# Performance work log

Hardware: AMD Instinct MI355X
Metric: run time of the kernel (lower is better)

Reference implementation:

```python
import jax, jax.numpy as jnp
import numpy as np

EPS = 1e-5
SCALE_MIN, SCALE_MAX = 0.6, 1.0


def _layer_norm(x):
    m = jnp.mean(x, axis=-1, keepdims=True)
    v = jnp.mean((x - m) ** 2, axis=-1, keepdims=True)
    return (x - m) / jnp.sqrt(v + EPS)


def _scan_dir(seq, A, Bp, Cp, D, W_in, W_out, snr_scale):
    """seq: [B, L, C] -> [B, L, C]. Diagonal SSM recurrence h = A*h + B*u."""
    Bsz, L, C = seq.shape
    N = A.shape[0]
    seq = _layer_norm(seq)
    u = jnp.einsum('blc,nc->bln', seq, W_in)                 # input_proj, [B,L,N]
    A_base = jnp.tanh(A)[None, :]                            # [1,N]
    s = jnp.clip(snr_scale, 0.0, 1.0)[:, None]               # [B,1]
    scale = SCALE_MIN + (SCALE_MAX - SCALE_MIN) * s
    Ad = jnp.clip(A_base * scale, -0.99, 0.99)               # [B,N]
    Bu = Bp[None, None, :] * u                               # [B,L,N]

    def step(h, bu_t):
        h = Ad * h + bu_t
        return h, h

    h0 = jnp.zeros((Bsz, N), dtype=seq.dtype)
    _, hs = jax.lax.scan(step, h0, jnp.swapaxes(Bu, 0, 1))   # hs: [L,B,N]
    hs = jnp.swapaxes(hs, 0, 1)                              # [B,L,N]
    y_state = Cp[None, None, :] * hs
    y = jnp.einsum('bln,cn->blc', y_state, W_out)            # output_proj
    return y + D[None, None, :] * seq


def _forward(x, snr_scale, A, Bparam, Cparam, D, W_in, W_out):
    Bsz, H, W, C = x.shape
    L = H * W
    if L > 4000:
        x = _layer_norm(x)
    # row scans
    seq_row = x.reshape(Bsz, L, C)
    y_row_f = _scan_dir(seq_row, A, Bparam, Cparam, D, W_in, W_out, snr_scale)
    y_row_b = _scan_dir(seq_row[:, ::-1, :], A, Bparam, Cparam, D, W_in, W_out, snr_scale)
    y_row = 0.5 * (y_row_f + y_row_b[:, ::-1, :])
    y_row = y_row.reshape(Bsz, H, W, C)
    # column scans
    x_col = jnp.transpose(x, (0, 2, 1, 3))                   # [B,W,H,C]
    seq_col = x_col.reshape(Bsz, L, C)
    y_col_f = _scan_dir(seq_col, A, Bparam, Cparam, D, W_in, W_out, snr_scale)
    y_col_b = _scan_dir(seq_col[:, ::-1, :], A, Bparam, Cparam, D, W_in, W_out, snr_scale)
    y_col = 0.5 * (y_col_f + y_col_b[:, ::-1, :])
    y_col = jnp.transpose(y_col.reshape(Bsz, W, H, C), (0, 2, 1, 3))
    return 0.5 * (y_row + y_col)


def setup_inputs() -> dict:
    key = jax.random.key(0)
    k = jax.random.split(key, 4)
    Bsz, H, W, C, N = 8, 64, 64, 256, 64
    x = jax.random.normal(k[0], (Bsz, H, W, C), dtype=jnp.float32)
    snr_scale = jax.random.uniform(k[1], (Bsz,), dtype=jnp.float32)
    A = -0.5 * jnp.ones((N,), dtype=jnp.float32)
    Bparam = 0.5 * jnp.ones((N,), dtype=jnp.float32)
    Cparam = 0.5 * jnp.ones((N,), dtype=jnp.float32)
    D = jnp.zeros((C,), dtype=jnp.float32)
    # nn.Linear default init: U(-1/sqrt(fan_in), 1/sqrt(fan_in))
    W_in = jax.random.uniform(k[2], (N, C), dtype=jnp.float32,
                              minval=-1.0 / np.sqrt(C), maxval=1.0 / np.sqrt(C))
    W_out = jax.random.uniform(k[3], (C, N), dtype=jnp.float32,
                               minval=-1.0 / np.sqrt(N), maxval=1.0 / np.sqrt(N))
    return {"x": x, "snr_scale": snr_scale, "A": A, "Bparam": Bparam,
            "Cparam": Cparam, "D": D, "W_in": W_in, "W_out": W_out}


def reference(x, snr_scale, A, Bparam, Cparam, D, W_in, W_out):
    return _forward(x, snr_scale, A, Bparam, Cparam, D, W_in, W_out)
```

## Files before the change

### kernel.cpp

```cpp
#include <hip/hip_runtime.h>
#include <hip/hip_bf16.h>
#include <math.h>

#define Bsz 8
#define Hh 64
#define Ww 64
#define Cc 256
#define Nn 64
#define Ll 4096
#define EPSf 1e-5f

typedef __bf16 v8bf __attribute__((ext_vector_type(8)));
typedef float  f32x4 __attribute__((ext_vector_type(4)));

__device__ __forceinline__ float ad_val(float a, float snr) {
    float s = fminf(fmaxf(snr, 0.f), 1.f);
    float scale = 0.6f + 0.4f * s;
    float v = tanhf(a) * scale;
    return fminf(fmaxf(v, -0.99f), 0.99f);
}

__global__ __launch_bounds__(256) void k0_weights(
    const float* __restrict__ Win, const float* __restrict__ Wout,
    const float* __restrict__ Bp, const float* __restrict__ Cp,
    __bf16* __restrict__ Wh, __bf16* __restrict__ Wl,
    __bf16* __restrict__ Woh, __bf16* __restrict__ Wol,
    float* __restrict__ WB)
{
    const int t = threadIdx.x;
    const int blk = blockIdx.x;
    if (blk < 4) {
        for (int idx = blk * 512 + t; idx < blk * 512 + 512; idx += 256) {
            int tile = idx >> 6, lane = idx & 63;
            int kt = tile >> 2, nt = tile & 3;
            int q = lane >> 4, n = nt * 16 + (lane & 15);
            #pragma unroll
            for (int j = 0; j < 8; ++j) {
                int k = kt * 32 + q * 8 + j;
                float w = Win[n * Cc + k];
                __bf16 h = (__bf16)w;
                Wh[idx * 8 + j] = h;
                Wl[idx * 8 + j] = (__bf16)(w - (float)h);
            }
        }
    } else if (blk < 8) {
        for (int idx = (blk - 4) * 512 + t; idx < (blk - 4) * 512 + 512; idx += 256) {
            int tile = idx >> 6, lane = idx & 63;
            int kt = tile >> 4, ntg = tile & 15;
            int q = lane >> 4, c = ntg * 16 + (lane & 15);
            #pragma unroll
            for (int j = 0; j < 8; ++j) {
                int k = kt * 32 + q * 8 + j;
                float w = Wout[c * Nn + k] * 0.25f * Cp[k];
                __bf16 h = (__bf16)w;
                Woh[idx * 8 + j] = h;
                Wol[idx * 8 + j] = (__bf16)(w - (float)h);
            }
        }
    } else {
        __shared__ float wtmp[256];
        int n = t >> 2, qd = t & 3;
        float s = 0.f;
        const float* wr = Win + (long)n * Cc + qd * 64;
        for (int i = 0; i < 64; ++i) s += wr[i];
        wtmp[t] = s;
        __syncthreads();
        if (t < 64)
            WB[t] = (wtmp[t*4] + wtmp[t*4+1] + wtmp[t*4+2] + wtmp[t*4+3]) * Bp[t];
    }
}

__global__ __launch_bounds__(256) void k1_ln_gemm(
    const float* __restrict__ x, const __bf16* __restrict__ Wh,
    const __bf16* __restrict__ Wl, const float* __restrict__ Bp,
    const float* __restrict__ WB, float* __restrict__ Bu,
    float* __restrict__ Mst, float* __restrict__ Sst)
{
    __shared__ float mrow[64], srow[64];
    const int t = threadIdx.x;
    const int lane = t & 63;
    const int wv = __builtin_amdgcn_readfirstlane(t >> 6);
    const long pbase = (long)blockIdx.x * 64;
    const float* xt = x + pbase * Cc;

    for (int rr = 0; rr < 16; ++rr) {
        int r = wv * 16 + rr;
        float4 v = ((const float4*)(xt + (long)r * Cc))[lane];
        float s = v.x + v.y + v.z + v.w;
        float q = v.x*v.x + v.y*v.y + v.z*v.z + v.w*v.w;
        #pragma unroll
        for (int off = 32; off > 0; off >>= 1) {
            s += __shfl_down(s, off);
            q += __shfl_down(q, off);
        }
        if (lane == 0) {
            float m = s * (1.f/256.f);
            float var = fmaxf(q * (1.f/256.f) - m*m, 0.f);
            float r1 = rsqrtf(var + EPSf);
            float v2 = var / (var + EPSf);
            float sc = r1 * rsqrtf(v2 + EPSf);
            mrow[r] = m; srow[r] = sc;
            Mst[pbase + r] = m; Sst[pbase + r] = sc;
        }
    }
    __syncthreads();

    const int q = lane >> 4;
    const int mi = lane & 15;
    const float* xa = xt + (long)(wv * 16 + mi) * Cc + q * 8;

    f32x4 acc[4];
    #pragma unroll
    for (int nt = 0; nt < 4; ++nt) acc[nt] = (f32x4){0.f, 0.f, 0.f, 0.f};

    #pragma unroll
    for (int kt = 0; kt < 8; ++kt) {
        float4 a0 = *(const float4*)(xa + kt * 32);
        float4 a1 = *(const float4*)(xa + kt * 32 + 4);
        float av[8] = {a0.x, a0.y, a0.z, a0.w, a1.x, a1.y, a1.z, a1.w};
        v8bf ah, al;
        #pragma unroll
        for (int j = 0; j < 8; ++j) {
            __bf16 h = (__bf16)av[j];
            ah[j] = h;
            al[j] = (__bf16)(av[j] - (float)h);
        }
        #pragma unroll
        for (int nt = 0; nt < 4; ++nt) {
            v8bf bh = *(const v8bf*)(Wh + ((long)(kt * 4 + nt) * 64 + lane) * 8);
            v8bf bl = *(const v8bf*)(Wl + ((long)(kt * 4 + nt) * 64 + lane) * 8);
            acc[nt] = __builtin_amdgcn_mfma_f32_16x16x32_bf16(ah, bh, acc[nt], 0, 0, 0);
            acc[nt] = __builtin_amdgcn_mfma_f32_16x16x32_bf16(al, bh, acc[nt], 0, 0, 0);
            acc[nt] = __builtin_amdgcn_mfma_f32_16x16x32_bf16(ah, bl, acc[nt], 0, 0, 0);
        }
    }

    #pragma unroll
    for (int nt = 0; nt < 4; ++nt) {
        int n = nt * 16 + mi;
        float bpn = Bp[n];
        float wbn = WB[n];
        #pragma unroll
        for (int reg = 0; reg < 4; ++reg) {
            int p = wv * 16 + q * 4 + reg;
            float m = mrow[p], s = srow[p];
            Bu[(pbase + p) * Nn + n] = s * (acc[nt][reg] * bpn - m * wbn);
        }
    }
}

__global__ __launch_bounds__(256) void k2_carry(
    const float* __restrict__ Bu, const float* __restrict__ A,
    const float* __restrict__ snr, float* __restrict__ E)
{
    const int t = threadIdx.x;
    const int lane = t & 63;
    const int task = blockIdx.x * 4 + (t >> 6);
    const int isCol = task >> 9;
    const int b = (task >> 6) & 7;
    const int j = task & 63;
    const float Ad = ad_val(A[lane], snr[b]);
    const float* src = Bu + ((long)b * Ll + (isCol ? j : j * 64)) * Nn + lane;
    const long stride = isCol ? (long)Ww * Nn : Nn;

    float v[64];
    #pragma unroll
    for (int k = 0; k < 64; ++k) v[k] = src[k * stride];

    float s = 0.f;
    #pragma unroll
    for (int k = 0; k < 64; ++k) s = fmaf(Ad, s, v[k]);
    const int dF = isCol ? 2 : 0;
    E[((dF * 8 + b) * 64 + j) * 64 + lane] = s;

    float sb = 0.f;
    #pragma unroll
    for (int k = 63; k >= 0; --k) sb = fmaf(Ad, sb, v[k]);
    E[(((dF + 1) * 8 + b) * 64 + (63 - j)) * 64 + lane] = sb;
}

__global__ __launch_bounds__(64) void k3_prefix(
    const float* __restrict__ E, float* __restrict__ CT,
    const float* __restrict__ A, const float* __restrict__ snr)
{
    const int lane = threadIdx.x;
    const int db = blockIdx.x;
    const int b = db & 7;
    float Ad = ad_val(A[lane], snr[b]);
    float p64 = Ad;
    #pragma unroll
    for (int i = 0; i < 6; ++i) p64 *= p64;
    const float* e = E + (long)db * 4096 + lane;
    float* ct = CT + (long)db * 4096 + lane;
    float v[64];
    #pragma unroll
    for (int k = 0; k < 64; ++k) v[k] = e[k * 64];
    float c = 0.f;
    #pragma unroll
    for (int k = 0; k < 64; ++k) {
        ct[k * 64] = c;
        c = fmaf(p64, c, v[k]);
    }
}

__global__ __launch_bounds__(256) void k4_apply(
    const float* __restrict__ Bu, const float* __restrict__ CT,
    const float* __restrict__ A, const float* __restrict__ snr,
    float* __restrict__ Srow, float* __restrict__ Scol)
{
    const int t = threadIdx.x;
    const int lane = t & 63;
    const int task = blockIdx.x * 4 + (t >> 6);
    const int isCol = task >> 9;
    const int b = (task >> 6) & 7;
    const int j = task & 63;
    const float Ad = ad_val(A[lane], snr[b]);
    const float* src = Bu + ((long)b * Ll + (isCol ? j : j * 64)) * Nn + lane;
    const long stride = isCol ? (long)Ww * Nn : Nn;
    const int dF = isCol ? 2 : 0;
    const float cf = CT[((dF * 8 + b) * 64 + j) * 64 + lane];
    const float cb = CT[(((dF + 1) * 8 + b) * 64 + (63 - j)) * 64 + lane];

    float v[64];
    #pragma unroll
    for (int k = 0; k < 64; ++k) v[k] = src[k * stride];

    float hf[64];
    float h = cf;
    #pragma unroll
    for (int k = 0; k < 64; ++k) { h = fmaf(Ad, h, v[k]); hf[k] = h; }

    float* out0 = (isCol ? Scol : Srow) +
                  ((long)b * Ll + (isCol ? j : j * 64)) * Nn + lane;
    float sb = cb;
    #pragma unroll
    for (int k = 63; k >= 0; --k) {
        sb = fmaf(Ad, sb, v[k]);
        out0[k * stride] = hf[k] + sb;
    }
}

__global__ __launch_bounds__(256) void k5_gemm_out(
    const float* __restrict__ Srow, const float* __restrict__ Scol,
    const float* __restrict__ x, const __bf16* __restrict__ Woh,
    const __bf16* __restrict__ Wol, const float* __restrict__ Dp,
    const float* __restrict__ Mst, const float* __restrict__ Sst,
    float* __restrict__ out)
{
    __shared__ float smem[64 * 260];
    const int t = threadIdx.x;
    const int lane = t & 63;
    const int wv = __builtin_amdgcn_readfirstlane(t >> 6);
    const long pbase = (long)blockIdx.x * 64;
    const int q = lane >> 4;
    const int mi = lane & 15;

    const float4* Sr = (const float4*)(Srow + pbase * Nn);
    const float4* Sc = (const float4*)(Scol + pbase * Nn);
    #pragma unroll
    for (int i = 0; i < 4; ++i) {
        int fi = i * 256 + t;
        float4 a = Sr[fi], c = Sc[fi];
        *(float4*)&smem[(fi >> 4) * 68 + (fi & 15) * 4] =
            make_float4(a.x + c.x, a.y + c.y, a.z + c.z, a.w + c.w);
    }
    __syncthreads();

    f32x4 acc[4][4];
    #pragma unroll
    for (int mt = 0; mt < 4; ++mt)
        #pragma unroll
        for (int nt = 0; nt < 4; ++nt) acc[mt][nt] = (f32x4){0.f, 0.f, 0.f, 0.f};

    #pragma unroll
    for (int kt = 0; kt < 2; ++kt) {
        v8bf bh[4], bl[4];
        #pragma unroll
        for (int nt = 0; nt < 4; ++nt) {
            long wo = ((long)(kt * 16 + wv * 4 + nt) * 64 + lane) * 8;
            bh[nt] = *(const v8bf*)(Woh + wo);
            bl[nt] = *(const v8bf*)(Wol + wo);
        }
        #pragma unroll
        for (int mt = 0; mt < 4; ++mt) {
            const float* ar = &smem[(mt * 16 + mi) * 68 + q * 8 + kt * 32];
            v8bf sh, sl;
            #pragma unroll
            for (int j = 0; j < 8; ++j) {
                float sv = ar[j];
                __bf16 hh = (__bf16)sv;
                sh[j] = hh;
                sl[j] = (__bf16)(sv - (float)hh);
            }
            #pragma unroll
            for (int nt = 0; nt < 4; ++nt) {
                acc[mt][nt] = __builtin_amdgcn_mfma_f32_16x16x32_bf16(sh, bh[nt], acc[mt][nt], 0, 0, 0);
                acc[mt][nt] = __builtin_amdgcn_mfma_f32_16x16x32_bf16(sl, bh[nt], acc[mt][nt], 0, 0, 0);
                acc[mt][nt] = __builtin_amdgcn_mfma_f32_16x16x32_bf16(sh, bl[nt], acc[mt][nt], 0, 0, 0);
            }
        }
    }
    __syncthreads();
    #pragma unroll
    for (int mt = 0; mt < 4; ++mt)
        #pragma unroll
        for (int nt = 0; nt < 4; ++nt) {
            int c = wv * 64 + nt * 16 + mi;
            #pragma unroll
            for (int reg = 0; reg < 4; ++reg)
                smem[(mt * 16 + q * 4 + reg) * 260 + c] = acc[mt][nt][reg];
        }
    __syncthreads();

    const float4* xg = (const float4*)(x + pbase * Cc);
    float4* og = (float4*)(out + pbase * Cc);
    const float4 dv = ((const float4*)Dp)[lane];
    #pragma unroll 4
    for (int i = 0; i < 16; ++i) {
        int fi = i * 256 + t;
        int p = i * 4 + wv;
        float4 v = *(const float4*)&smem[p * 260 + lane * 4];
        float m = Mst[pbase + p], s = Sst[pbase + p];
        float4 xv = xg[fi];
        og[fi] = make_float4(v.x + dv.x * ((xv.x - m) * s),
                             v.y + dv.y * ((xv.y - m) * s),
                             v.z + dv.z * ((xv.z - m) * s),
                             v.w + dv.w * ((xv.w - m) * s));
    }
}

extern "C" void kernel_launch(void* const* d_in, const int* in_sizes, int n_in,
                              void* d_out, int out_size, void* d_ws, size_t ws_size,
                              hipStream_t stream)
{
    const float* x    = (const float*)d_in[0];
    const float* snr  = (const float*)d_in[1];
    const float* A    = (const float*)d_in[2];
    const float* Bp   = (const float*)d_in[3];
    const float* Cp   = (const float*)d_in[4];
    const float* Dp   = (const float*)d_in[5];
    const float* Win  = (const float*)d_in[6];
    const float* Wout = (const float*)d_in[7];
    float* out = (float*)d_out;

    char* ws = (char*)d_ws;
    float*  Bu   = (float*)(ws);
    float*  Srow = (float*)(ws + (size_t)8  * 1024 * 1024);
    float*  Scol = (float*)(ws + (size_t)16 * 1024 * 1024);
    float*  E    = (float*)(ws + (size_t)24 * 1024 * 1024);
    float*  CT   = (float*)(ws + (size_t)24 * 1024 * 1024 + 512*1024);
    float*  Mst  = (float*)(ws + (size_t)25 * 1024 * 1024);
    float*  Sst  = (float*)(ws + (size_t)25 * 1024 * 1024 + 128*1024);
    char*   wbase = ws + (size_t)25 * 1024 * 1024 + 512 * 1024;
    __bf16* Wh   = (__bf16*)(wbase);
    __bf16* Wl   = (__bf16*)(wbase + 32 * 1024);
    __bf16* Woh  = (__bf16*)(wbase + 64 * 1024);
    __bf16* Wol  = (__bf16*)(wbase + 96 * 1024);
    float*  WB   = (float*)(wbase + 128 * 1024);

    hipLaunchKernelGGL(k0_weights,  dim3(9),   dim3(256), 0, stream, Win, Wout, Bp, Cp, Wh, Wl, Woh, Wol, WB);
    hipLaunchKernelGGL(k1_ln_gemm,  dim3(512), dim3(256), 0, stream, x, Wh, Wl, Bp, WB, Bu, Mst, Sst);
    hipLaunchKernelGGL(k2_carry,    dim3(256), dim3(256), 0, stream, Bu, A, snr, E);
    hipLaunchKernelGGL(k3_prefix,   dim3(32),  dim3(64),  0, stream, E, CT, A, snr);
    hipLaunchKernelGGL(k4_apply,    dim3(256), dim3(256), 0, stream, Bu, CT, A, snr, Srow, Scol);
    hipLaunchKernelGGL(k5_gemm_out, dim3(512), dim3(256), 0, stream, Srow, Scol, x, Woh, Wol, Dp, Mst, Sst, out);
}
```

Before: 140.8 us.

## Fuse row-scan carry into LN-GEMM and row-scan apply into output GEMM

Row-direction scan chunk carries are now computed inside k1 from the Bu tile held in LDS, using a 4-segment split per 64-row chunk. The row-direction apply is moved into k5, which rebuilds the row scan from Bu plus the prefix carries and adds the column result before the output GEMM. This removes the Srow buffer and its 8 MB write and read, and halves the k2 and k4 grids to column-only work. In exchange k1 and k5 take extra LDS, barriers and sequential per-segment recurrence work.

```diff
diff --git a/kernel.cpp b/kernel.cpp
--- a/kernel.cpp
+++ b/kernel.cpp
@@ -73,10 +73,14 @@
 __global__ __launch_bounds__(256) void k1_ln_gemm(
     const float* __restrict__ x, const __bf16* __restrict__ Wh,
     const __bf16* __restrict__ Wl, const float* __restrict__ Bp,
-    const float* __restrict__ WB, float* __restrict__ Bu,
+    const float* __restrict__ WB, const float* __restrict__ A,
+    const float* __restrict__ snr,
+    float* __restrict__ Bu, float* __restrict__ E,
     float* __restrict__ Mst, float* __restrict__ Sst)
 {
     __shared__ float mrow[64], srow[64];
+    __shared__ float tile[64 * 68];
+    __shared__ float pfs[4][64], pbs[4][64];
     const int t = threadIdx.x;
     const int lane = t & 63;
     const int wv = __builtin_amdgcn_readfirstlane(t >> 6);
@@ -144,8 +148,44 @@
         for (int reg = 0; reg < 4; ++reg) {
             int p = wv * 16 + q * 4 + reg;
             float m = mrow[p], s = srow[p];
-            Bu[(pbase + p) * Nn + n] = s * (acc[nt][reg] * bpn - m * wbn);
-        }
+            float val = s * (acc[nt][reg] * bpn - m * wbn);
+            Bu[(pbase + p) * Nn + n] = val;
+            tile[p * 68 + n] = val;
+        }
+    }
+    __syncthreads();
+
+    const int nn = t & 63;
+    const int seg = t >> 6;
+    const int bb = blockIdx.x >> 6;
+    const int jj = blockIdx.x & 63;
+    const float Adv = ad_val(A[nn], snr[bb]);
+
+    float vv[16];
+    #pragma unroll
+    for (int k = 0; k < 16; ++k) vv[k] = tile[(seg * 16 + k) * 68 + nn];
+    float f = 0.f, bw = 0.f;
+    #pragma unroll
+    for (int k = 0; k < 16; ++k) f = fmaf(Adv, f, vv[k]);
+    #pragma unroll
+    for (int k = 15; k >= 0; --k) bw = fmaf(Adv, bw, vv[k]);
+    pfs[seg][nn] = f;
+    pbs[seg][nn] = bw;
+    __syncthreads();
+
+    if (t < 64) {
+        float Ad16 = Adv * Adv;
+        Ad16 *= Ad16;
+        Ad16 *= Ad16;
+        Ad16 *= Ad16;
+        float cf = pfs[0][t];
+        #pragma unroll
+        for (int i = 1; i < 4; ++i) cf = fmaf(Ad16, cf, pfs[i][t]);
+        E[((0 * 8 + bb) * 64 + jj) * 64 + t] = cf;
+        float cb = pbs[3][t];
+        #pragma unroll
+        for (int i = 2; i >= 0; --i) cb = fmaf(Ad16, cb, pbs[i][t]);
+        E[((1 * 8 + bb) * 64 + (63 - jj)) * 64 + t] = cb;
     }
 }
 
@@ -156,12 +196,11 @@
     const int t = threadIdx.x;
     const int lane = t & 63;
     const int task = blockIdx.x * 4 + (t >> 6);
-    const int isCol = task >> 9;
     const int b = (task >> 6) & 7;
     const int j = task & 63;
     const float Ad = ad_val(A[lane], snr[b]);
-    const float* src = Bu + ((long)b * Ll + (isCol ? j : j * 64)) * Nn + lane;
-    const long stride = isCol ? (long)Ww * Nn : Nn;
+    const float* src = Bu + ((long)b * Ll + j) * Nn + lane;
+    const long stride = (long)Ww * Nn;
 
     float v[64];
     #pragma unroll
@@ -170,13 +209,12 @@
     float s = 0.f;
     #pragma unroll
     for (int k = 0; k < 64; ++k) s = fmaf(Ad, s, v[k]);
-    const int dF = isCol ? 2 : 0;
-    E[((dF * 8 + b) * 64 + j) * 64 + lane] = s;
+    E[((2 * 8 + b) * 64 + j) * 64 + lane] = s;
 
     float sb = 0.f;
     #pragma unroll
     for (int k = 63; k >= 0; --k) sb = fmaf(Ad, sb, v[k]);
-    E[(((dF + 1) * 8 + b) * 64 + (63 - j)) * 64 + lane] = sb;
+    E[((3 * 8 + b) * 64 + (63 - j)) * 64 + lane] = sb;
 }
 
 __global__ __launch_bounds__(64) void k3_prefix(
@@ -206,20 +244,18 @@
 __global__ __launch_bounds__(256) void k4_apply(
     const float* __restrict__ Bu, const float* __restrict__ CT,
     const float* __restrict__ A, const float* __restrict__ snr,
-    float* __restrict__ Srow, float* __restrict__ Scol)
+    float* __restrict__ Scol)
 {
     const int t = threadIdx.x;
     const int lane = t & 63;
     const int task = blockIdx.x * 4 + (t >> 6);
-    const int isCol = task >> 9;
     const int b = (task >> 6) & 7;
     const int j = task & 63;
     const float Ad = ad_val(A[lane], snr[b]);
-    const float* src = Bu + ((long)b * Ll + (isCol ? j : j * 64)) * Nn + lane;
-    const long stride = isCol ? (long)Ww * Nn : Nn;
-    const int dF = isCol ? 2 : 0;
-    const float cf = CT[((dF * 8 + b) * 64 + j) * 64 + lane];
-    const float cb = CT[(((dF + 1) * 8 + b) * 64 + (63 - j)) * 64 + lane];
+    const float* src = Bu + ((long)b * Ll + j) * Nn + lane;
+    const long stride = (long)Ww * Nn;
+    const float cf = CT[((2 * 8 + b) * 64 + j) * 64 + lane];
+    const float cb = CT[((3 * 8 + b) * 64 + (63 - j)) * 64 + lane];
 
     float v[64];
     #pragma unroll
@@ -230,8 +266,7 @@
     #pragma unroll
     for (int k = 0; k < 64; ++k) { h = fmaf(Ad, h, v[k]); hf[k] = h; }
 
-    float* out0 = (isCol ? Scol : Srow) +
-                  ((long)b * Ll + (isCol ? j : j * 64)) * Nn + lane;
+    float* out0 = Scol + ((long)b * Ll + j) * Nn + lane;
     float sb = cb;
     #pragma unroll
     for (int k = 63; k >= 0; --k) {
@@ -241,13 +276,16 @@
 }
 
 __global__ __launch_bounds__(256) void k5_gemm_out(
-    const float* __restrict__ Srow, const float* __restrict__ Scol,
+    const float* __restrict__ Bu, const float* __restrict__ Scol,
+    const float* __restrict__ CT, const float* __restrict__ A,
+    const float* __restrict__ snr,
     const float* __restrict__ x, const __bf16* __restrict__ Woh,
     const __bf16* __restrict__ Wol, const float* __restrict__ Dp,
     const float* __restrict__ Mst, const float* __restrict__ Sst,
     float* __restrict__ out)
 {
     __shared__ float smem[64 * 260];
+    __shared__ float pfs[4][64], pbs[4][64];
     const int t = threadIdx.x;
     const int lane = t & 63;
     const int wv = __builtin_amdgcn_readfirstlane(t >> 6);
@@ -255,14 +293,54 @@
     const int q = lane >> 4;
     const int mi = lane & 15;
 
-    const float4* Sr = (const float4*)(Srow + pbase * Nn);
-    const float4* Sc = (const float4*)(Scol + pbase * Nn);
+    const float4* Bg = (const float4*)(Bu + pbase * Nn);
     #pragma unroll
     for (int i = 0; i < 4; ++i) {
         int fi = i * 256 + t;
-        float4 a = Sr[fi], c = Sc[fi];
-        *(float4*)&smem[(fi >> 4) * 68 + (fi & 15) * 4] =
-            make_float4(a.x + c.x, a.y + c.y, a.z + c.z, a.w + c.w);
+        float4 a = Bg[fi];
+        *(float4*)&smem[(fi >> 4) * 68 + (fi & 15) * 4] = a;
+    }
+    __syncthreads();
+
+    const int nn = t & 63;
+    const int seg = t >> 6;
+    const int bb = blockIdx.x >> 6;
+    const int jj = blockIdx.x & 63;
+    const float Adv = ad_val(A[nn], snr[bb]);
+    float Ad16 = Adv * Adv; Ad16 *= Ad16; Ad16 *= Ad16; Ad16 *= Ad16;
+    const float cf  = CT[((0 * 8 + bb) * 64 + jj) * 64 + nn];
+    const float cbg = CT[((1 * 8 + bb) * 64 + (63 - jj)) * 64 + nn];
+
+    float vv[16], sc[16];
+    #pragma unroll
+    for (int k = 0; k < 16; ++k) vv[k] = smem[(seg * 16 + k) * 68 + nn];
+    const float* scp = Scol + (pbase + seg * 16) * Nn + nn;
+    #pragma unroll
+    for (int k = 0; k < 16; ++k) sc[k] = scp[k * 64];
+
+    float f = 0.f, bw = 0.f;
+    #pragma unroll
+    for (int k = 0; k < 16; ++k) f = fmaf(Adv, f, vv[k]);
+    #pragma unroll
+    for (int k = 15; k >= 0; --k) bw = fmaf(Adv, bw, vv[k]);
+    pfs[seg][nn] = f;
+    pbs[seg][nn] = bw;
+    __syncthreads();
+
+    float hseed = cf;
+    for (int i = 0; i < seg; ++i) hseed = fmaf(Ad16, hseed, pfs[i][nn]);
+    float bseed = cbg;
+    for (int i = 3; i > seg; --i) bseed = fmaf(Ad16, bseed, pbs[i][nn]);
+
+    float hf[16];
+    float h = hseed;
+    #pragma unroll
+    for (int k = 0; k < 16; ++k) { h = fmaf(Adv, h, vv[k]); hf[k] = h; }
+    float sb = bseed;
+    #pragma unroll
+    for (int k = 15; k >= 0; --k) {
+        sb = fmaf(Adv, sb, vv[k]);
+        smem[(seg * 16 + k) * 68 + nn] = hf[k] + sb + sc[k];
     }
     __syncthreads();
 
@@ -345,13 +423,12 @@
 
     char* ws = (char*)d_ws;
     float*  Bu   = (float*)(ws);
-    float*  Srow = (float*)(ws + (size_t)8  * 1024 * 1024);
-    float*  Scol = (float*)(ws + (size_t)16 * 1024 * 1024);
-    float*  E    = (float*)(ws + (size_t)24 * 1024 * 1024);
-    float*  CT   = (float*)(ws + (size_t)24 * 1024 * 1024 + 512*1024);
-    float*  Mst  = (float*)(ws + (size_t)25 * 1024 * 1024);
-    float*  Sst  = (float*)(ws + (size_t)25 * 1024 * 1024 + 128*1024);
-    char*   wbase = ws + (size_t)25 * 1024 * 1024 + 512 * 1024;
+    float*  Scol = (float*)(ws + (size_t)8  * 1024 * 1024);
+    float*  E    = (float*)(ws + (size_t)16 * 1024 * 1024);
+    float*  CT   = (float*)(ws + (size_t)16 * 1024 * 1024 + 512*1024);
+    float*  Mst  = (float*)(ws + (size_t)17 * 1024 * 1024);
+    float*  Sst  = (float*)(ws + (size_t)17 * 1024 * 1024 + 128*1024);
+    char*   wbase = ws + (size_t)17 * 1024 * 1024 + 512 * 1024;
     __bf16* Wh   = (__bf16*)(wbase);
     __bf16* Wl   = (__bf16*)(wbase + 32 * 1024);
     __bf16* Woh  = (__bf16*)(wbase + 64 * 1024);
@@ -359,9 +436,9 @@
     float*  WB   = (float*)(wbase + 128 * 1024);
 
     hipLaunchKernelGGL(k0_weights,  dim3(9),   dim3(256), 0, stream, Win, Wout, Bp, Cp, Wh, Wl, Woh, Wol, WB);
-    hipLaunchKernelGGL(k1_ln_gemm,  dim3(512), dim3(256), 0, stream, x, Wh, Wl, Bp, WB, Bu, Mst, Sst);
-    hipLaunchKernelGGL(k2_carry,    dim3(256), dim3(256), 0, stream, Bu, A, snr, E);
+    hipLaunchKernelGGL(k1_ln_gemm,  dim3(512), dim3(256), 0, stream, x, Wh, Wl, Bp, WB, A, snr, Bu, E, Mst, Sst);
+    hipLaunchKernelGGL(k2_carry,    dim3(128), dim3(256), 0, stream, Bu, A, snr, E);
     hipLaunchKernelGGL(k3_prefix,   dim3(32),  dim3(64),  0, stream, E, CT, A, snr);
-    hipLaunchKernelGGL(k4_apply,    dim3(256), dim3(256), 0, stream, Bu, CT, A, snr, Srow, Scol);
-    hipLaunchKernelGGL(k5_gemm_out, dim3(512), dim3(256), 0, stream, Srow, Scol, x, Woh, Wol, Dp, Mst, Sst, out);
-}
+    hipLaunchKernelGGL(k4_apply,    dim3(128), dim3(256), 0, stream, Bu, CT, A, snr, Scol);
+    hipLaunchKernelGGL(k5_gemm_out, dim3(512), dim3(256), 0, stream, Bu, Scol, CT, A, snr, x, Woh, Wol, Dp, Mst, Sst, out);
+}
```

Result: faster. 138.0 us (-2.0%).
